# Kernel tuning notes

Hardware: AMD Instinct MI355X
Metric: run time of the kernel (lower is better)

The kernel has to match this reference:

```python
import jax, jax.numpy as jnp
import numpy as np

ROWS, COLS = 4096, 2048
NUM_BITS = 4
NUM_LEVELS = 2 ** NUM_BITS  # 16
FIXED_T = 100.0
EPS = 1e-06


def setup_inputs() -> dict:
    key = jax.random.key(0)
    kw, = jax.random.split(key, 1)
    weight = jax.random.normal(kw, (ROWS, COLS), dtype=jnp.float32)
    col_min = weight.min(axis=0)
    col_max = weight.max(axis=0)
    pad = 0.01 * (col_max - col_min)
    w_min = col_min - pad  # [COLS]
    w_max = col_max + pad  # [COLS]
    return {"weight": weight, "w_min": w_min, "w_max": w_max}


def reference(weight, w_min, w_max):
    # Torch clamps against the *detached scalar* of the other bound -> stop_gradient
    w_min_c = jnp.minimum(w_min, jax.lax.stop_gradient(w_max) - EPS)          # [C]
    w_max_c = jnp.maximum(w_max, jax.lax.stop_gradient(w_min_c) + EPS)        # [C]
    rng = w_max_c - w_min_c                                                   # [C]

    q_levels = jnp.linspace(0.0, 1.0, NUM_LEVELS, dtype=weight.dtype)         # [L]

    w_norm = (weight - w_min_c[None, :]) / (rng[None, :] + EPS)               # [R, C]
    dists = -jnp.abs(w_norm[:, :, None] - q_levels[None, None, :])            # [R, C, L]
    soft_probs = jax.nn.softmax(dists * FIXED_T, axis=-1)                     # [R, C, L]

    w_q = jnp.einsum("rcl,l->rc", soft_probs, q_levels)                       # [R, C]
    w_dequant = w_q * rng[None, :] + w_min_c[None, :]                         # [R, C]

    bin_mass = soft_probs.sum(axis=0)                                         # [C, L]
    bin_probs = bin_mass / (bin_mass.sum(axis=-1, keepdims=True) + EPS)       # [C, L]
    entropy_per_col = -(bin_probs * jnp.log(bin_probs + EPS)).sum(axis=-1)    # [C]
    total_entropy = entropy_per_col.sum()

    return (w_dequant, total_entropy)
```

## Files before the change

kernel.cpp:

```cpp
#include <hip/hip_runtime.h>

#define ROWS 4096
#define COLS 2048
#define NLEV 16
#define TEMP 100.0f
#define EPS  1e-6f
#define LOG2E 1.4426950408889634f
#define RGEO 1.2726356e-3f

#define TPB 128
#define RPB 32
#define RBLKS (ROWS / RPB)
#define UNROLL 8

typedef _Float16 half8_t __attribute__((ext_vector_type(8)));
typedef _Float16 half2_t __attribute__((ext_vector_type(2)));


__global__ __launch_bounds__(TPB) void quant_main_kernel(
    const float* __restrict__ weight,
    const float* __restrict__ w_min,
    const float* __restrict__ w_max,
    float* __restrict__ dequant,
    _Float16* __restrict__ partial,
    float* __restrict__ out_ent)
{
    __shared__ float bins[34 * TPB];

    const int t  = threadIdx.x;
    const int c  = blockIdx.x * TPB + t;
    const int r0 = blockIdx.y * RPB;

    if (blockIdx.x == 0 && blockIdx.y == 0 && t == 0) out_ent[0] = 0.0f;

#pragma unroll
    for (int l = 0; l < 34; ++l) bins[l * TPB + t] = 0.0f;

    const float wmin = w_min[c];
    const float wmax = w_max[c];
    const float mn   = fminf(wmin, wmax - EPS);
    const float mx   = fmaxf(wmax, mn + EPS);
    const float rng  = mx - mn;
    const float inv_rng = __builtin_amdgcn_rcpf(rng + EPS);

    const float S     = (TEMP / 15.0f) * LOG2E;
    const float invS  = 15.0f / (TEMP * LOG2E);
    const float scale = inv_rng * (TEMP * LOG2E);
    const float zb    = -mn * scale;
    const float rng15 = rng * (1.0f / 15.0f);

    const float* __restrict__ wp = weight  + (size_t)r0 * COLS + c;
    float* __restrict__       dq = dequant + (size_t)r0 * COLS + c;

    for (int r = 0; r < RPB; r += UNROLL) {
        float w[UNROLL];
#pragma unroll
        for (int j = 0; j < UNROLL; ++j)
            w[j] = wp[(size_t)(r + j) * COLS];

#pragma unroll
        for (int j = 0; j < UNROLL; ++j) {
            const float z  = fmaf(w[j], scale, zb);
            float kf = floorf(z * invS);
            kf = fminf(fmaxf(kf, 0.0f), 14.0f);
            const int ki = (int)kf;
            const float f = fmaf(-kf, S, z);

            const float t_ = __builtin_amdgcn_exp2f(-fabsf(f));
            const float u_ = __builtin_amdgcn_exp2f(-fabsf(f - S));
            const float e1 = (kf >= 1.0f)  ? RGEO : 0.0f;
            const float e2 = (kf <= 13.0f) ? RGEO : 0.0f;
            const float t1 = t_ * e1;
            const float u2 = u_ * e2;
            const float s  = (t_ + t1) + (u_ + u2);
            const float inv_s = __builtin_amdgcn_rcpf(s);
            const float ws = fmaf(kf, s, u_) + fmaf(2.0f, u2, -t1);

            dq[(size_t)(r + j) * COLS] = fmaf(ws * inv_s, rng15, mn);

            const int base = ki * TPB + t;
            bins[base           ] += t_ * inv_s;
            bins[base + 19 * TPB] += u_ * inv_s;
        }
    }

    float a[17], b[17];
#pragma unroll
    for (int l = 0; l < 17; ++l) a[l] = bins[l * TPB + t];
#pragma unroll
    for (int l = 0; l < 17; ++l) b[l] = bins[(17 + l) * TPB + t];

    half8_t v0, v1;
#pragma unroll
    for (int l = 0; l < 16; ++l) {
        const float bin = (a[l] + b[l + 1]) + RGEO * (a[l + 1] + b[l]);
        if (l < 8) v0[l] = (_Float16)bin; else v1[l - 8] = (_Float16)bin;
    }
    half8_t* pp = (half8_t*)(partial + ((size_t)blockIdx.y * COLS + c) * NLEV);
    pp[0] = v0;
    pp[1] = v1;
}

__global__ __launch_bounds__(256) void reduce_entropy_kernel(
    const _Float16* __restrict__ partial,
    float* __restrict__ out_ent)
{
    __shared__ float red[256];
    const int i = blockIdx.x * 256 + threadIdx.x;
    const half2_t* p2 = (const half2_t*)partial;

    float m0 = 0.0f, m1 = 0.0f;
#pragma unroll 4
    for (int rb = 0; rb < RBLKS; ++rb) {
        const half2_t v = p2[(size_t)rb * (COLS * NLEV / 2) + i];
        m0 += (float)v[0];
        m1 += (float)v[1];
    }

    float tot = m0 + m1;
    tot += __shfl_xor(tot, 1);
    tot += __shfl_xor(tot, 2);
    tot += __shfl_xor(tot, 4);
    const float inv = __builtin_amdgcn_rcpf(tot + EPS);

    const float p0 = m0 * inv;
    const float p1 = m1 * inv;
    float ent = -(p0 * __logf(p0 + EPS) + p1 * __logf(p1 + EPS));

    red[threadIdx.x] = ent;
    __syncthreads();
#pragma unroll
    for (int off = 128; off > 0; off >>= 1) {
        if (threadIdx.x < off) red[threadIdx.x] += red[threadIdx.x + off];
        __syncthreads();
    }
    if (threadIdx.x == 0) atomicAdd(out_ent, red[0]);
}

extern "C" void kernel_launch(void* const* d_in, const int* in_sizes, int n_in,
                              void* d_out, int out_size, void* d_ws, size_t ws_size,
                              hipStream_t stream)
{
    const float* weight = (const float*)d_in[0];
    const float* w_min  = (const float*)d_in[1];
    const float* w_max  = (const float*)d_in[2];

    float* out     = (float*)d_out;
    float* dequant = out;
    float* out_ent = out + (size_t)ROWS * COLS;
    _Float16* partial = (_Float16*)d_ws;

    quant_main_kernel<<<dim3(COLS / TPB, RBLKS), TPB, 0, stream>>>(
        weight, w_min, w_max, dequant, partial, out_ent);

    reduce_entropy_kernel<<<(COLS * NLEV / 2) / 256, 256, 0, stream>>>(
        partial, out_ent);
}
```

Baseline: 100.2 us.

## Simplify two-level softmax math and use LDS atomics for bin accumulation

Drops the abs and the geometric edge-correction terms from the per-element softmax. Approximate coefficients (C1P/C2P) are folded into the weighted-sum numerator, while the histogram accumulates only the two nearest-level probabilities, using LDS atomic adds into a 16-bin shared array instead of 34 bins plus a post-combine. Block size grows from 128 to 256 threads, and the smaller shared footprint allows more resident blocks. This cuts ALU work and LDS size per element. The trade-off is lower accuracy for the neighbour-bin mass contributions, plus atomic serialization cost in LDS.

Result: slower. 173.4 us (+73.1%).

```diff
diff --git a/kernel.cpp b/kernel.cpp
--- a/kernel.cpp
+++ b/kernel.cpp
@@ -6,9 +6,11 @@
 #define TEMP 100.0f
 #define EPS  1e-6f
 #define LOG2E 1.4426950408889634f
-#define RGEO 1.2726356e-3f
+#define RGEO 1.2726338e-3f
+#define C2P  1.2710160e-3f
+#define C1P  (1.0f + C2P)
 
-#define TPB 128
+#define TPB 256
 #define RPB 32
 #define RBLKS (ROWS / RPB)
 #define UNROLL 8
@@ -25,7 +27,7 @@
     _Float16* __restrict__ partial,
     float* __restrict__ out_ent)
 {
-    __shared__ float bins[34 * TPB];
+    __shared__ float bins[16 * TPB];
 
     const int t  = threadIdx.x;
     const int c  = blockIdx.x * TPB + t;
@@ -34,7 +36,7 @@
     if (blockIdx.x == 0 && blockIdx.y == 0 && t == 0) out_ent[0] = 0.0f;
 
 #pragma unroll
-    for (int l = 0; l < 34; ++l) bins[l * TPB + t] = 0.0f;
+    for (int l = 0; l < 16; ++l) bins[l * TPB + t] = 0.0f;
 
     const float wmin = w_min[c];
     const float wmax = w_max[c];
@@ -61,39 +63,30 @@
 #pragma unroll
         for (int j = 0; j < UNROLL; ++j) {
             const float z  = fmaf(w[j], scale, zb);
-            float kf = floorf(z * invS);
+            const float y  = z * invS;
+            float kf = floorf(y);
             kf = fminf(fmaxf(kf, 0.0f), 14.0f);
             const int ki = (int)kf;
             const float f = fmaf(-kf, S, z);
 
-            const float t_ = __builtin_amdgcn_exp2f(-fabsf(f));
-            const float u_ = __builtin_amdgcn_exp2f(-fabsf(f - S));
-            const float e1 = (kf >= 1.0f)  ? RGEO : 0.0f;
-            const float e2 = (kf <= 13.0f) ? RGEO : 0.0f;
-            const float t1 = t_ * e1;
-            const float u2 = u_ * e2;
-            const float s  = (t_ + t1) + (u_ + u2);
-            const float inv_s = __builtin_amdgcn_rcpf(s);
-            const float ws = fmaf(kf, s, u_) + fmaf(2.0f, u2, -t1);
+            const float t_ = __builtin_amdgcn_exp2f(-f);
+            const float u_ = __builtin_amdgcn_exp2f(f - S);
+            const float sum0 = t_ + u_;
+            const float inv  = __builtin_amdgcn_rcpf(sum0);
+            const float ws = fmaf(kf, sum0, fmaf(u_, C1P, -(C2P * t_)));
 
-            dq[(size_t)(r + j) * COLS] = fmaf(ws * inv_s, rng15, mn);
+            dq[(size_t)(r + j) * COLS] = fmaf(ws * inv, rng15, mn);
 
             const int base = ki * TPB + t;
-            bins[base           ] += t_ * inv_s;
-            bins[base + 19 * TPB] += u_ * inv_s;
+            unsafeAtomicAdd(&bins[base],       t_ * inv);
+            unsafeAtomicAdd(&bins[base + TPB], u_ * inv);
         }
     }
-
-    float a[17], b[17];
-#pragma unroll
-    for (int l = 0; l < 17; ++l) a[l] = bins[l * TPB + t];
-#pragma unroll
-    for (int l = 0; l < 17; ++l) b[l] = bins[(17 + l) * TPB + t];
 
     half8_t v0, v1;
 #pragma unroll
     for (int l = 0; l < 16; ++l) {
-        const float bin = (a[l] + b[l + 1]) + RGEO * (a[l + 1] + b[l]);
+        const float bin = bins[l * TPB + t];
         if (l < 8) v0[l] = (_Float16)bin; else v1[l - 8] = (_Float16)bin;
     }
     half8_t* pp = (half8_t*)(partial + ((size_t)blockIdx.y * COLS + c) * NLEV);
```
